# Optimization experiments

Measured on AMD Instinct MI355X. Metric: run time of the kernel, lower is better.

The kernel has to match this reference:

```python
import jax, jax.numpy as jnp
import numpy as np

D_MODEL = 1024
N_HEADS = 16
CHUNK = 64
EPS = 1e-6


def elu_plus_1(x):
    return jax.nn.elu(x) + 1.0


def setup_inputs() -> dict:
    key = jax.random.key(0)
    kx, kq, kk, kv, ko = jax.random.split(key, 5)
    B, T = 4, 4096
    # xavier_uniform for square (D, D) weights: limit = sqrt(6/(D+D))
    lim = float(np.sqrt(6.0 / (D_MODEL + D_MODEL)))
    mk = lambda k: jax.random.uniform(k, (D_MODEL, D_MODEL), jnp.float32, -lim, lim)
    return {
        "x": jax.random.normal(kx, (B, T, D_MODEL), jnp.float32),
        "W_q": mk(kq),
        "W_k": mk(kk),
        "W_v": mk(kv),
        "W_o": mk(ko),
    }


def reference(x, W_q, W_k, W_v, W_o):
    B, T, D = x.shape
    H = N_HEADS
    dk = D // H
    dv = dk
    C = CHUNK
    N = T // C  # T chosen divisible by chunk size (no padding needed)

    q = (x @ W_q.T).reshape(B, T, H, dk)
    k = (x @ W_k.T).reshape(B, T, H, dk)
    v = (x @ W_v.T).reshape(B, T, H, dv)

    phi_q = elu_plus_1(q).reshape(B, N, C, H, dk)
    phi_k = elu_plus_1(k).reshape(B, N, C, H, dk)
    vc = v.reshape(B, N, C, H, dv)

    # Per-chunk key-value outer products and key sums, then exclusive prefix
    # sums over chunks give the carried state S and normalizer z at each
    # chunk's start (same math as the sequential chunk loop).
    KV = jnp.einsum('bnchk,bnchv->bnhkv', phi_k, vc)      # (B,N,H,dk,dv)
    Ksum = phi_k.sum(axis=2)                               # (B,N,C->sum,H,dk) -> (B,N,H,dk)
    KV_cum = jnp.cumsum(KV, axis=1)
    Ksum_cum = jnp.cumsum(Ksum, axis=1)
    S_prefix = jnp.concatenate([jnp.zeros_like(KV_cum[:, :1]), KV_cum[:, :-1]], axis=1)
    z_prefix = jnp.concatenate([jnp.zeros_like(Ksum_cum[:, :1]), Ksum_cum[:, :-1]], axis=1)

    # Inter-chunk contribution from carried state
    inter = jnp.einsum('bnchk,bnhkv->bnchv', phi_q, S_prefix)   # (B,N,C,H,dv)
    z_inter = jnp.einsum('bnchk,bnhk->bnch', phi_q, z_prefix)   # (B,N,C,H)

    # Intra-chunk causal attention
    mask = jnp.tril(jnp.ones((C, C), dtype=x.dtype))
    attn = jnp.einsum('bnihk,bnjhk->bnhij', phi_q, phi_k) * mask  # (B,N,H,C,C)
    intra = jnp.einsum('bnhij,bnjhv->bnihv', attn, vc)            # (B,N,C,H,dv)
    z_intra = attn.sum(axis=-1).transpose(0, 1, 3, 2)             # (B,N,C,H)

    denom = jnp.clip((z_inter + z_intra)[..., None], 1e-6, None)
    y = (inter + intra) / denom                                   # (B,N,C,H,dv)
    y = y.reshape(B, T, H * dv)
    return y @ W_o.T
```

## Files before the change

### kernel.cpp

```cpp
#include <hip/hip_runtime.h>


typedef unsigned short u16;
typedef float  f32x4 __attribute__((ext_vector_type(4)));
typedef short  b16x8 __attribute__((ext_vector_type(8)));
typedef u16    u16x4 __attribute__((ext_vector_type(4)));
typedef u16    u16x8 __attribute__((ext_vector_type(8)));

#define DEVINL __device__ __forceinline__

DEVINL u16 f2b(float f) {
  unsigned u = __float_as_uint(f);
  return (u16)((u + 0x7fffu + ((u >> 16) & 1u)) >> 16);
}
DEVINL float b2f(u16 s) { return __uint_as_float(((unsigned)s) << 16); }

DEVINL f32x4 mfma16(b16x8 a, b16x8 b, f32x4 c) {
  return __builtin_amdgcn_mfma_f32_16x16x32_bf16(a, b, c, 0, 0, 0);
}

DEVINL float phi_elu1(float v) { return v > 0.f ? v + 1.f : __expf(v); }

__global__ void cvt_kernel(const float* __restrict__ in, u16* __restrict__ out, int n8) {
  int stride = gridDim.x * blockDim.x;
  for (int i = blockIdx.x * blockDim.x + threadIdx.x; i < n8; i += stride) {
    const float* p = in + (size_t)i * 8;
    f32x4 a = *(const f32x4*)p;
    f32x4 b = *(const f32x4*)(p + 4);
    u16x8 o;
    o[0] = f2b(a[0]); o[1] = f2b(a[1]); o[2] = f2b(a[2]); o[3] = f2b(a[3]);
    o[4] = f2b(b[0]); o[5] = f2b(b[1]); o[6] = f2b(b[2]); o[7] = f2b(b[3]);
    *(u16x8*)(out + (size_t)i * 8) = o;
  }
}

template <bool PHI, typename OT>
__global__ __launch_bounds__(256, 2) void gemm_bt(const u16* __restrict__ A,
                                                  const u16* __restrict__ B,
                                                  OT* __restrict__ C, int M, int N) {
  __shared__ char lds[32768];
  const int tid = threadIdx.x, wid = tid >> 6, l = tid & 63;
  const int l15 = l & 15, lg = l >> 4;
  const int ntn = N >> 7;
  const int nwg = gridDim.x, bid = blockIdx.x;
  const int cpx = nwg >> 3;
  const int sb = (bid & 7) * cpx + (bid >> 3);
  const int tm = sb / ntn, tn = sb - tm * ntn;
  const int wr = wid >> 1, wc = wid & 1;

  f32x4 acc[4][4];
#pragma unroll
  for (int i = 0; i < 4; i++)
#pragma unroll
    for (int j = 0; j < 4; j++) acc[i][j] = f32x4{0.f, 0.f, 0.f, 0.f};

  const u16* sptr[8];
#pragma unroll
  for (int i = 0; i < 8; i++) {
    int sidx = wid * 8 + i;
    int o = sidx * 1024 + l * 16;
    int lo = o & 16383;
    int row = lo >> 7;
    int cb = (lo & 127) ^ ((row & 7) << 4);
    sptr[i] = (o < 16384 ? A + (size_t)(tm * 128 + row) * 1024
                         : B + (size_t)(tn * 128 + row) * 1024) + (cb >> 1);
  }

  for (int kt = 0; kt < 16; ++kt) {
    const int k0 = kt * 64;
#pragma unroll
    for (int i = 0; i < 8; i++) {
      __builtin_amdgcn_global_load_lds(
          (const __attribute__((address_space(1))) void*)(sptr[i] + k0),
          (__attribute__((address_space(3))) void*)(lds + (wid * 8 + i) * 1024),
          16, 0, 0);
    }
    __syncthreads();
#pragma unroll
    for (int ks = 0; ks < 2; ++ks) {
      b16x8 af[4], bf[4];
#pragma unroll
      for (int fm = 0; fm < 4; ++fm) {
        int row = wr * 64 + fm * 16 + l15;
        af[fm] = *(const b16x8*)(lds + row * 128 + ((ks * 64 + lg * 16) ^ ((row & 7) << 4)));
      }
#pragma unroll
      for (int fn = 0; fn < 4; ++fn) {
        int row = wc * 64 + fn * 16 + l15;
        bf[fn] = *(const b16x8*)(lds + 16384 + row * 128 + ((ks * 64 + lg * 16) ^ ((row & 7) << 4)));
      }
#pragma unroll
      for (int fm = 0; fm < 4; ++fm)
#pragma unroll
        for (int fn = 0; fn < 4; ++fn) acc[fm][fn] = mfma16(af[fm], bf[fn], acc[fm][fn]);
    }
    __syncthreads();
  }

#pragma unroll
  for (int fm = 0; fm < 4; ++fm)
#pragma unroll
    for (int fn = 0; fn < 4; ++fn)
#pragma unroll
      for (int r = 0; r < 4; ++r) {
        size_t grow = tm * 128 + wr * 64 + fm * 16 + lg * 4 + r;
        size_t gcol = tn * 128 + wc * 64 + fn * 16 + l15;
        float v = acc[fm][fn][r];
        if (PHI) v = phi_elu1(v);
        OT* p = C + grow * (size_t)N + gcol;
        if constexpr (sizeof(OT) == 2) *p = (OT)f2b(v);
        else                           *p = (OT)v;
      }
}

__global__ __launch_bounds__(256) void transpose64(const u16* __restrict__ in,
                                                   u16* __restrict__ out) {
  __shared__ u16 tile[64][68];
  const int t = threadIdx.x;
  const int tr = blockIdx.x, tc = blockIdx.y;
#pragma unroll
  for (int i = 0; i < 4; i++) {
    int idx = i * 256 + t, r = idx >> 4, c4 = idx & 15;
    u16x4 v = *(const u16x4*)(in + (size_t)(tr * 64 + r) * 1024 + tc * 64 + c4 * 4);
    *(u16x4*)&tile[r][c4 * 4] = v;
  }
  __syncthreads();
#pragma unroll
  for (int i = 0; i < 4; i++) {
    int idx = i * 256 + t, oc = idx >> 4, r4 = idx & 15;
    u16x4 v;
    v[0] = tile[r4 * 4 + 0][oc]; v[1] = tile[r4 * 4 + 1][oc];
    v[2] = tile[r4 * 4 + 2][oc]; v[3] = tile[r4 * 4 + 3][oc];
    *(u16x4*)(out + (size_t)(tc * 64 + oc) * 16384 + tr * 64 + r4 * 4) = v;
  }
}

__global__ __launch_bounds__(256, 2) void kv_kernel(const u16* __restrict__ kT,
                                                    const u16* __restrict__ vT,
                                                    u16* __restrict__ KVT,
                                                    float* __restrict__ Ksum) {
  const int tid = threadIdx.x, wid = tid >> 6, l = tid & 63, l15 = l & 15, lg = l >> 4;
  const int bid = blockIdx.x, hg = bid & 3, bn = bid >> 2, n = bn & 63, b = bn >> 6;
  const int h = hg * 4 + wid;
  const size_t cb = (size_t)b * 4096 + n * 64 + lg * 8;

  b16x8 af[4][2], bf[4][2];
#pragma unroll
  for (int fm = 0; fm < 4; fm++)
#pragma unroll
    for (int ks = 0; ks < 2; ks++)
      af[fm][ks] = *(const b16x8*)(vT + (size_t)(h * 64 + fm * 16 + l15) * 16384 + cb + ks * 32);
#pragma unroll
  for (int fn = 0; fn < 4; fn++)
#pragma unroll
    for (int ks = 0; ks < 2; ks++)
      bf[fn][ks] = *(const b16x8*)(kT + (size_t)(h * 64 + fn * 16 + l15) * 16384 + cb + ks * 32);

  f32x4 acc[4][4];
#pragma unroll
  for (int i = 0; i < 4; i++)
#pragma unroll
    for (int j = 0; j < 4; j++) acc[i][j] = f32x4{0.f, 0.f, 0.f, 0.f};
#pragma unroll
  for (int ks = 0; ks < 2; ks++)
#pragma unroll
    for (int fm = 0; fm < 4; fm++)
#pragma unroll
      for (int fn = 0; fn < 4; fn++) acc[fm][fn] = mfma16(af[fm][ks], bf[fn][ks], acc[fm][fn]);

  float ksum[4] = {0.f, 0.f, 0.f, 0.f};
#pragma unroll
  for (int fn = 0; fn < 4; fn++) {
#pragma unroll
    for (int ks = 0; ks < 2; ks++)
#pragma unroll
      for (int j = 0; j < 8; j++) ksum[fn] += b2f((u16)bf[fn][ks][j]);
    ksum[fn] += __shfl_xor(ksum[fn], 16);
    ksum[fn] += __shfl_xor(ksum[fn], 32);
  }
  const size_t ob = (size_t)(b * 64 + n) * 16 + h;
  if (l < 16) {
#pragma unroll
    for (int fn = 0; fn < 4; fn++) Ksum[ob * 64 + fn * 16 + l15] = ksum[fn];
  }
#pragma unroll
  for (int fm = 0; fm < 4; fm++)
#pragma unroll
    for (int fn = 0; fn < 4; fn++)
#pragma unroll
      for (int r = 0; r < 4; r++)
        KVT[ob * 4096 + (size_t)(fm * 16 + lg * 4 + r) * 64 + fn * 16 + l15] =
            f2b(acc[fm][fn][r]);
}

__global__ __launch_bounds__(256) void scan_s(const u16* __restrict__ KVT,
                                              u16* __restrict__ ST) {
  const int bh = blockIdx.x >> 4, slice = blockIdx.x & 15;
  const int b = bh >> 4, h = bh & 15;
  const int e = slice * 256 + threadIdx.x;
  float acc = 0.f;
  for (int n = 0; n < 64; n++) {
    size_t idx = ((size_t)(b * 64 + n) * 16 + h) * 4096 + e;
    ST[idx] = f2b(acc);
    acc += b2f(KVT[idx]);
  }
}

__global__ __launch_bounds__(64) void scan_z(const float* __restrict__ Ksum,
                                             float* __restrict__ zpre) {
  const int b = blockIdx.x >> 4, h = blockIdx.x & 15;
  const int t = threadIdx.x;
  float acc = 0.f;
  for (int n = 0; n < 64; n++) {
    size_t idx = ((size_t)(b * 64 + n) * 16 + h) * 64 + t;
    zpre[idx] = acc;
    acc += Ksum[idx];
  }
}

__global__ __launch_bounds__(256, 2) void attn_out(const u16* __restrict__ phiQ,
                                                   const u16* __restrict__ phiK,
                                                   const u16* __restrict__ vT,
                                                   const u16* __restrict__ ST,
                                                   const float* __restrict__ zpre,
                                                   u16* __restrict__ Y) {
  __shared__ char lds[4 * 8192 + 4 * 256];
  const int tid = threadIdx.x, wid = tid >> 6, l = tid & 63, l15 = l & 15, lg = l >> 4;
  const int bid = blockIdx.x, hg = bid & 3, bn = bid >> 2, n = bn & 63, b = bn >> 6;
  const int h = hg * 4 + wid;
  const size_t row0 = (size_t)b * 4096 + n * 64;
  const int dcol = h * 64;

  b16x8 qf[4][2];
#pragma unroll
  for (int fi = 0; fi < 4; fi++)
#pragma unroll
    for (int ks = 0; ks < 2; ks++)
      qf[fi][ks] = *(const b16x8*)(phiQ + (row0 + fi * 16 + l15) * 1024 + dcol + lg * 8 + ks * 32);

  f32x4 accT[4][4];
#pragma unroll
  for (int i = 0; i < 4; i++)
#pragma unroll
    for (int j = 0; j < 4; j++) accT[i][j] = f32x4{0.f, 0.f, 0.f, 0.f};
  {
    b16x8 kf[4][2];
#pragma unroll
    for (int fj = 0; fj < 4; fj++)
#pragma unroll
      for (int ks = 0; ks < 2; ks++)
        kf[fj][ks] = *(const b16x8*)(phiK + (row0 + fj * 16 + l15) * 1024 + dcol + lg * 8 + ks * 32);
#pragma unroll
    for (int ks = 0; ks < 2; ks++)
#pragma unroll
      for (int fj = 0; fj < 4; fj++)
#pragma unroll
        for (int fi = 0; fi < 4; fi++)
          accT[fj][fi] = mfma16(kf[fj][ks], qf[fi][ks], accT[fj][fi]);
  }

  const size_t zb = ((size_t)(b * 64 + n) * 16 + h) * 64;
  float zi[4] = {0.f, 0.f, 0.f, 0.f};
#pragma unroll
  for (int ks = 0; ks < 2; ks++) {
    f32x4 z0 = *(const f32x4*)(zpre + zb + lg * 8 + ks * 32);
    f32x4 z1 = *(const f32x4*)(zpre + zb + lg * 8 + ks * 32 + 4);
#pragma unroll
    for (int fi = 0; fi < 4; fi++)
#pragma unroll
      for (int j = 0; j < 4; j++) {
        zi[fi] += b2f((u16)qf[fi][ks][j])     * z0[j];
        zi[fi] += b2f((u16)qf[fi][ks][j + 4]) * z1[j];
      }
  }

  char* abuf = lds + wid * 8192;
  float zt[4] = {0.f, 0.f, 0.f, 0.f};
#pragma unroll
  for (int fi = 0; fi < 4; fi++) {
    const int i = fi * 16 + l15;
    const int swz = (i & 7) << 4;
#pragma unroll
    for (int fj = 0; fj < 4; fj++) {
      f32x4 v = accT[fj][fi];
#pragma unroll
      for (int r = 0; r < 4; r++) {
        int j = fj * 16 + lg * 4 + r;
        if (j > i) v[r] = 0.f;
        zt[fi] += v[r];
      }
      unsigned w0 = (unsigned)f2b(v[0]) | ((unsigned)f2b(v[1]) << 16);
      unsigned w1 = (unsigned)f2b(v[2]) | ((unsigned)f2b(v[3]) << 16);
      int jb = (fj * 16 + lg * 4) * 2;
      *(unsigned*)(abuf + i * 128 + (jb ^ swz)) = w0;
      *(unsigned*)(abuf + i * 128 + ((jb + 4) ^ swz)) = w1;
    }
  }

  float* dbuf = (float*)(lds + 32768 + wid * 256);
#pragma unroll
  for (int fi = 0; fi < 4; fi++) {
    float z = zi[fi] + zt[fi];
    z += __shfl_xor(z, 16);
    z += __shfl_xor(z, 32);
    float rd = 1.f / fmaxf(z, 1e-6f);
    if (l < 16) dbuf[fi * 16 + l15] = rd;
  }
  __syncthreads();

  b16x8 stf[4][2], vf[4][2];
  const size_t stb = ((size_t)(b * 64 + n) * 16 + h) * 4096;
#pragma unroll
  for (int fn = 0; fn < 4; fn++)
#pragma unroll
    for (int ks = 0; ks < 2; ks++) {
      stf[fn][ks] = *(const b16x8*)(ST + stb + (size_t)(fn * 16 + l15) * 64 + lg * 8 + ks * 32);
      vf[fn][ks]  = *(const b16x8*)(vT + (size_t)(dcol + fn * 16 + l15) * 16384 +
                                    (size_t)b * 4096 + n * 64 + lg * 8 + ks * 32);
    }
  f32x4 acc[4][4];
#pragma unroll
  for (int i = 0; i < 4; i++)
#pragma unroll
    for (int j = 0; j < 4; j++) acc[i][j] = f32x4{0.f, 0.f, 0.f, 0.f};
#pragma unroll
  for (int ks = 0; ks < 2; ks++)
#pragma unroll
    for (int fm = 0; fm < 4; fm++)
#pragma unroll
      for (int fn = 0; fn < 4; fn++) acc[fm][fn] = mfma16(qf[fm][ks], stf[fn][ks], acc[fm][fn]);
#pragma unroll
  for (int fm = 0; fm < 4; fm++) {
    const int i = fm * 16 + l15;
    const int swz = (i & 7) << 4;
#pragma unroll
    for (int ks = 0; ks < 2; ks++) {
      b16x8 af = *(const b16x8*)(abuf + i * 128 + ((ks * 64 + lg * 16) ^ swz));
#pragma unroll
      for (int fn = 0; fn < 4; fn++) acc[fm][fn] = mfma16(af, vf[fn][ks], acc[fm][fn]);
    }
  }

#pragma unroll
  for (int fm = 0; fm < 4; fm++)
#pragma unroll
    for (int r = 0; r < 4; r++) {
      float rd = dbuf[fm * 16 + lg * 4 + r];
#pragma unroll
      for (int fn = 0; fn < 4; fn++)
        Y[(row0 + fm * 16 + lg * 4 + r) * 1024 + dcol + fn * 16 + l15] =
            f2b(acc[fm][fn][r] * rd);
    }
}

extern "C" void kernel_launch(void* const* d_in, const int* in_sizes, int n_in,
                              void* d_out, int out_size, void* d_ws, size_t ws_size,
                              hipStream_t stream) {
  const float* x  = (const float*)d_in[0];
  const float* Wq = (const float*)d_in[1];
  const float* Wk = (const float*)d_in[2];
  const float* Wv = (const float*)d_in[3];
  const float* Wo = (const float*)d_in[4];
  float* out = (float*)d_out;

  char* ws = (char*)d_ws;
  size_t off = 0;
  auto alloc = [&](size_t bytes) -> char* {
    char* p = ws + off;
    off += (bytes + 255) & ~(size_t)255;
    return p;
  };
  u16*   xb   = (u16*)alloc(33554432);
  u16*   wqb  = (u16*)alloc(2097152);
  u16*   wkb  = (u16*)alloc(2097152);
  u16*   wvb  = (u16*)alloc(2097152);
  u16*   wob  = (u16*)alloc(2097152);
  u16*   phiQ = (u16*)alloc(33554432);
  u16*   phiK = (u16*)alloc(33554432);
  u16*   vT   = (u16*)alloc(33554432);
  u16*   kT   = (u16*)alloc(33554432);
  u16*   KVT  = (u16*)alloc(33554432);
  float* Ksum = (float*)alloc(1048576);
  u16*   ST   = (u16*)alloc(33554432);
  float* zpre = (float*)alloc(1048576);
  u16*   y    = xb;

  cvt_kernel<<<2048, 256, 0, stream>>>(x, xb, 2097152);
  cvt_kernel<<<512, 256, 0, stream>>>(Wq, wqb, 131072);
  cvt_kernel<<<512, 256, 0, stream>>>(Wk, wkb, 131072);
  cvt_kernel<<<512, 256, 0, stream>>>(Wv, wvb, 131072);
  cvt_kernel<<<512, 256, 0, stream>>>(Wo, wob, 131072);

  gemm_bt<true, u16><<<1024, 256, 0, stream>>>(xb, wqb, phiQ, 16384, 1024);
  gemm_bt<true, u16><<<1024, 256, 0, stream>>>(xb, wkb, phiK, 16384, 1024);
  gemm_bt<false, u16><<<1024, 256, 0, stream>>>(wvb, xb, vT, 1024, 16384);

  transpose64<<<dim3(256, 16), 256, 0, stream>>>(phiK, kT);
  kv_kernel<<<1024, 256, 0, stream>>>(kT, vT, KVT, Ksum);
  scan_s<<<1024, 256, 0, stream>>>(KVT, ST);
  scan_z<<<64, 64, 0, stream>>>(Ksum, zpre);
  attn_out<<<1024, 256, 0, stream>>>(phiQ, phiK, vT, ST, zpre, y);

  gemm_bt<false, float><<<1024, 256, 0, stream>>>(y, wob, out, 16384, 1024);
}
```

Baseline: 269.0 us.

## Replace GEMM with 256x256-tile, 8-wave double-buffered pipelined kernel

Replaces the 128x128 single-buffered GEMM with a 256x256 tile kernel using 512 threads and 128KB of double-buffered LDS. Global-to-LDS loads for the next k-step are staged in quarters, interleaved with four MFMA phases that use setprio and barriers. This raises data reuse per tile and overlaps memory traffic with compute. In exchange it launches only 256 workgroups, which may leave some CUs underused, and the large LDS footprint limits occupancy.

```diff
diff --git a/kernel.cpp b/kernel.cpp
--- a/kernel.cpp
+++ b/kernel.cpp
@@ -35,76 +35,127 @@
 }
 
 template <bool PHI, typename OT>
-__global__ __launch_bounds__(256, 2) void gemm_bt(const u16* __restrict__ A,
+__global__ __launch_bounds__(512, 2) void gemm256(const u16* __restrict__ A,
                                                   const u16* __restrict__ B,
                                                   OT* __restrict__ C, int M, int N) {
-  __shared__ char lds[32768];
+  __shared__ char lds[131072];
   const int tid = threadIdx.x, wid = tid >> 6, l = tid & 63;
   const int l15 = l & 15, lg = l >> 4;
-  const int ntn = N >> 7;
+  const int wr = wid >> 2, wc = wid & 3;
+  const int ntn = N >> 8;
   const int nwg = gridDim.x, bid = blockIdx.x;
   const int cpx = nwg >> 3;
   const int sb = (bid & 7) * cpx + (bid >> 3);
   const int tm = sb / ntn, tn = sb - tm * ntn;
-  const int wr = wid >> 1, wc = wid & 1;
-
-  f32x4 acc[4][4];
-#pragma unroll
-  for (int i = 0; i < 4; i++)
+
+  const int colX0 = (lg * 16) ^ ((l15 & 7) << 4);
+  const int colX1 = (64 + lg * 16) ^ ((l15 & 7) << 4);
+  char* ldsA = lds + wr * 16384 + l15 * 128;
+  char* ldsB = lds + 32768 + (wc >> 1) * 16384 + ((wc & 1) * 64 + l15) * 128;
+
+  const int srow = tid >> 3;
+  const int scol = ((((tid & 7) * 16) ^ ((srow & 7) << 4)) >> 1);
+  const u16* sA = A + (size_t)(tm * 256 + srow) * 1024 + scol;
+  const u16* sB = B + (size_t)(tn * 256 + srow) * 1024 + scol;
+  char* ldsStage = lds + wid * 1024;
+
+#define STAGE(tt, h)                                                            \
+  do {                                                                          \
+    const u16* s_ = ((h) < 2 ? sA : sB) + (size_t)(((h) & 1) * 128) * 1024 +    \
+                    (size_t)(tt) * 64;                                          \
+    char* d_ = ldsStage + (((tt) & 1) << 16) + ((h) < 2 ? 0 : 32768) +          \
+               (((h) & 1) << 14);                                               \
+    __builtin_amdgcn_global_load_lds(                                           \
+        (const __attribute__((address_space(1))) void*)(s_),                    \
+        (__attribute__((address_space(3))) void*)(d_), 16, 0, 0);               \
+    __builtin_amdgcn_global_load_lds(                                           \
+        (const __attribute__((address_space(1))) void*)(s_ + 64 * 1024),        \
+        (__attribute__((address_space(3))) void*)(d_ + 8192), 16, 0, 0);        \
+  } while (0)
+
+  f32x4 acc[8][4];
+#pragma unroll
+  for (int i = 0; i < 8; i++)
 #pragma unroll
     for (int j = 0; j < 4; j++) acc[i][j] = f32x4{0.f, 0.f, 0.f, 0.f};
 
-  const u16* sptr[8];
-#pragma unroll
-  for (int i = 0; i < 8; i++) {
-    int sidx = wid * 8 + i;
-    int o = sidx * 1024 + l * 16;
-    int lo = o & 16383;
-    int row = lo >> 7;
-    int cb = (lo & 127) ^ ((row & 7) << 4);
-    sptr[i] = (o < 16384 ? A + (size_t)(tm * 128 + row) * 1024
-                         : B + (size_t)(tn * 128 + row) * 1024) + (cb >> 1);
-  }
-
-  for (int kt = 0; kt < 16; ++kt) {
-    const int k0 = kt * 64;
-#pragma unroll
-    for (int i = 0; i < 8; i++) {
-      __builtin_amdgcn_global_load_lds(
-          (const __attribute__((address_space(1))) void*)(sptr[i] + k0),
-          (__attribute__((address_space(3))) void*)(lds + (wid * 8 + i) * 1024),
-          16, 0, 0);
-    }
-    __syncthreads();
-#pragma unroll
-    for (int ks = 0; ks < 2; ++ks) {
-      b16x8 af[4], bf[4];
-#pragma unroll
-      for (int fm = 0; fm < 4; ++fm) {
-        int row = wr * 64 + fm * 16 + l15;
-        af[fm] = *(const b16x8*)(lds + row * 128 + ((ks * 64 + lg * 16) ^ ((row & 7) << 4)));
-      }
-#pragma unroll
-      for (int fn = 0; fn < 4; ++fn) {
-        int row = wc * 64 + fn * 16 + l15;
-        bf[fn] = *(const b16x8*)(lds + 16384 + row * 128 + ((ks * 64 + lg * 16) ^ ((row & 7) << 4)));
-      }
-#pragma unroll
-      for (int fm = 0; fm < 4; ++fm)
-#pragma unroll
-        for (int fn = 0; fn < 4; ++fn) acc[fm][fn] = mfma16(af[fm], bf[fn], acc[fm][fn]);
-    }
-    __syncthreads();
-  }
-
-#pragma unroll
-  for (int fm = 0; fm < 4; ++fm)
+  STAGE(0, 0); STAGE(0, 1); STAGE(0, 2); STAGE(0, 3);
+  STAGE(1, 2); STAGE(1, 3);
+  asm volatile("s_waitcnt vmcnt(4)" ::: "memory");
+  __builtin_amdgcn_s_barrier();
+
+  b16x8 a0[4], a1[4], b0[4], b1[4];
+  for (int t = 0; t < 16; ++t) {
+    const int cb = (t & 1) << 16;
+#pragma unroll
+    for (int fm = 0; fm < 4; fm++) a0[fm] = *(const b16x8*)(ldsA + cb + fm * 2048 + colX0);
+#pragma unroll
+    for (int fn = 0; fn < 4; fn++) b0[fn] = *(const b16x8*)(ldsB + cb + fn * 2048 + colX0);
+    if (t < 15) STAGE(t + 1, 0);
+    __builtin_amdgcn_s_barrier();
+    asm volatile("s_waitcnt lgkmcnt(0)" ::: "memory");
+    __builtin_amdgcn_sched_barrier(0);
+    __builtin_amdgcn_s_setprio(1);
+#pragma unroll
+    for (int fm = 0; fm < 4; fm++)
+#pragma unroll
+      for (int fn = 0; fn < 4; fn++) acc[fm][fn] = mfma16(a0[fm], b0[fn], acc[fm][fn]);
+    __builtin_amdgcn_s_setprio(0);
+    __builtin_amdgcn_s_barrier();
+#pragma unroll
+    for (int fm = 0; fm < 4; fm++) a1[fm] = *(const b16x8*)(ldsA + cb + (4 + fm) * 2048 + colX0);
+#pragma unroll
+    for (int fn = 0; fn < 4; fn++) b1[fn] = *(const b16x8*)(ldsB + cb + fn * 2048 + colX1);
+    if (t < 15) STAGE(t + 1, 1);
+    __builtin_amdgcn_s_barrier();
+    asm volatile("s_waitcnt lgkmcnt(0)" ::: "memory");
+    __builtin_amdgcn_sched_barrier(0);
+    __builtin_amdgcn_s_setprio(1);
+#pragma unroll
+    for (int fm = 0; fm < 4; fm++)
+#pragma unroll
+      for (int fn = 0; fn < 4; fn++) acc[4 + fm][fn] = mfma16(a1[fm], b0[fn], acc[4 + fm][fn]);
+    __builtin_amdgcn_s_setprio(0);
+    __builtin_amdgcn_s_barrier();
+#pragma unroll
+    for (int fm = 0; fm < 4; fm++) a0[fm] = *(const b16x8*)(ldsA + cb + fm * 2048 + colX1);
+    if (t < 14) STAGE(t + 2, 2);
+    __builtin_amdgcn_s_barrier();
+    asm volatile("s_waitcnt lgkmcnt(0)" ::: "memory");
+    __builtin_amdgcn_sched_barrier(0);
+    __builtin_amdgcn_s_setprio(1);
+#pragma unroll
+    for (int fm = 0; fm < 4; fm++)
+#pragma unroll
+      for (int fn = 0; fn < 4; fn++) acc[fm][fn] = mfma16(a0[fm], b1[fn], acc[fm][fn]);
+    __builtin_amdgcn_s_setprio(0);
+    __builtin_amdgcn_s_barrier();
+#pragma unroll
+    for (int fm = 0; fm < 4; fm++) a1[fm] = *(const b16x8*)(ldsA + cb + (4 + fm) * 2048 + colX1);
+    if (t < 14) STAGE(t + 2, 3);
+    __builtin_amdgcn_s_barrier();
+    asm volatile("s_waitcnt lgkmcnt(0)" ::: "memory");
+    __builtin_amdgcn_sched_barrier(0);
+    __builtin_amdgcn_s_setprio(1);
+#pragma unroll
+    for (int fm = 0; fm < 4; fm++)
+#pragma unroll
+      for (int fn = 0; fn < 4; fn++) acc[4 + fm][fn] = mfma16(a1[fm], b1[fn], acc[4 + fm][fn]);
+    __builtin_amdgcn_s_setprio(0);
+    if (t < 14) asm volatile("s_waitcnt vmcnt(4)" ::: "memory");
+    else        asm volatile("s_waitcnt vmcnt(0)" ::: "memory");
+    __builtin_amdgcn_s_barrier();
+  }
+#undef STAGE
+
+#pragma unroll
+  for (int fm = 0; fm < 8; ++fm)
 #pragma unroll
     for (int fn = 0; fn < 4; ++fn)
 #pragma unroll
       for (int r = 0; r < 4; ++r) {
-        size_t grow = tm * 128 + wr * 64 + fm * 16 + lg * 4 + r;
-        size_t gcol = tn * 128 + wc * 64 + fn * 16 + l15;
+        size_t grow = (size_t)tm * 256 + wr * 128 + fm * 16 + lg * 4 + r;
+        size_t gcol = (size_t)tn * 256 + wc * 64 + fn * 16 + l15;
         float v = acc[fm][fn][r];
         if (PHI) v = phi_elu1(v);
         OT* p = C + grow * (size_t)N + gcol;
@@ -391,9 +442,9 @@
   cvt_kernel<<<512, 256, 0, stream>>>(Wv, wvb, 131072);
   cvt_kernel<<<512, 256, 0, stream>>>(Wo, wob, 131072);
 
-  gemm_bt<true, u16><<<1024, 256, 0, stream>>>(xb, wqb, phiQ, 16384, 1024);
-  gemm_bt<true, u16><<<1024, 256, 0, stream>>>(xb, wkb, phiK, 16384, 1024);
-  gemm_bt<false, u16><<<1024, 256, 0, stream>>>(wvb, xb, vT, 1024, 16384);
+  gemm256<true, u16><<<256, 512, 0, stream>>>(xb, wqb, phiQ, 16384, 1024);
+  gemm256<true, u16><<<256, 512, 0, stream>>>(xb, wkb, phiK, 16384, 1024);
+  gemm256<false, u16><<<256, 512, 0, stream>>>(wvb, xb, vT, 1024, 16384);
 
   transpose64<<<dim3(256, 16), 256, 0, stream>>>(phiK, kT);
   kv_kernel<<<1024, 256, 0, stream>>>(kT, vT, KVT, Ksum);
@@ -401,5 +452,5 @@
   scan_z<<<64, 64, 0, stream>>>(Ksum, zpre);
   attn_out<<<1024, 256, 0, stream>>>(phiQ, phiK, vT, ST, zpre, y);
 
-  gemm_bt<false, float><<<1024, 256, 0, stream>>>(y, wob, out, 16384, 1024);
-}
+  gemm256<false, float><<<256, 512, 0, stream>>>(y, wob, out, 16384, 1024);
+}
```

After: 252.3 us. 1.07x faster.
